# Performance work log

Hardware: AMD Instinct MI355X
Metric: run time of the kernel (lower is better)

## Reference

```python
import jax, jax.numpy as jnp
import numpy as np
import math

B, S, D = 8, 4096, 768
H = 12
DH = D // H  # attention_head_size = 64


def setup_inputs() -> dict:
    key = jax.random.key(0)
    ks = jax.random.split(key, 6)
    sc = 0.02
    return {
        "hidden_states": jax.random.normal(ks[0], (B, S, D), dtype=jnp.float32),
        "attention_mask": jnp.zeros((B, 1, S), dtype=jnp.float32),
        "Wq": jax.random.normal(ks[1], (D, D), dtype=jnp.float32) * sc,
        "bq": jnp.zeros((D,), dtype=jnp.float32),
        "Wqa": jax.random.normal(ks[2], (H, D), dtype=jnp.float32) * sc,
        "bqa": jnp.zeros((H,), dtype=jnp.float32),
        "Wk": jax.random.normal(ks[3], (D, D), dtype=jnp.float32) * sc,
        "bk": jnp.zeros((D,), dtype=jnp.float32),
        "Wt": jax.random.normal(ks[4], (D, D), dtype=jnp.float32) * sc,
        "bt": jnp.zeros((D,), dtype=jnp.float32),
    }


def reference(hidden_states, attention_mask, Wq, bq, Wqa, bqa, Wk, bk, Wt, bt):
    inv_sqrt_dh = 1.0 / math.sqrt(DH)
    # projections (torch nn.Linear: x @ W.T + b)
    q = hidden_states @ Wq.T + bq            # [B,S,D]
    k = hidden_states @ Wk.T + bk            # [B,S,D]
    # query attention logits -> [B,H,S]
    qfs = jnp.swapaxes(q @ Wqa.T + bqa, 1, 2) * inv_sqrt_dh + attention_mask
    qw = jax.nn.softmax(qfs, axis=-1)        # [B,H,S]
    ql = jnp.swapaxes(q.reshape(B, S, H, DH), 1, 2)  # [B,H,S,DH]
    kl = jnp.swapaxes(k.reshape(B, S, H, DH), 1, 2)  # [B,H,S,DH]
    # global pooled query per head
    pooled_q = jnp.einsum('bhs,bhsd->bhd', qw, ql)   # [B,H,DH]
    # key attention over pooled query
    qks = jnp.einsum('bhsd,bhd->bhs', kl, pooled_q) * inv_sqrt_dh + attention_mask
    qkw = jax.nn.softmax(qks, axis=-1)       # [B,H,S]
    pooled_k = jnp.einsum('bhs,bhsd->bhd', qkw, kl)  # [B,H,DH]
    # gate query with pooled key, merge heads
    wv = pooled_k[:, :, None, :] * ql        # [B,H,S,DH]
    wv = jnp.swapaxes(wv, 1, 2).reshape(B, S, D)
    return wv @ Wt.T + bt + q
```

## Files before the change

kernel.cpp:

```cpp
#include <hip/hip_runtime.h>
#include <cstdint>
#include <cstddef>

#define S_LEN 4096
#define NB 8
#define NH 12
#define DMODEL 768
#define DHEAD 64
#define M_TOT (NB * S_LEN)
#define INV_SQRT_DH 0.125f
#define WSZ (DMODEL * DMODEL)

typedef __attribute__((ext_vector_type(4))) float f32x4;
typedef __attribute__((ext_vector_type(8))) short bf16x8;

__device__ inline float bf2f(unsigned short h) {
    union { unsigned int u; float f; } v; v.u = ((unsigned int)h) << 16; return v.f;
}
__device__ inline unsigned short f2bf(float f) {
    union { float f; unsigned int u; } v; v.f = f;
    unsigned int r = v.u + 0x7FFFu + ((v.u >> 16) & 1u);
    return (unsigned short)(r >> 16);
}

__device__ inline void gload_lds16(const unsigned short* gp, void* lp) {
    __builtin_amdgcn_global_load_lds((const __attribute__((address_space(1))) void*)gp,
                                     (__attribute__((address_space(3))) void*)lp,
                                     16, 0, 0);
}

__global__ void prep_all(const float* __restrict__ hs,
                         const float* __restrict__ Wq, const float* __restrict__ Wk,
                         const float* __restrict__ Wt, const float* __restrict__ Wqa,
                         const float* __restrict__ bq, const float* __restrict__ bk,
                         unsigned short* __restrict__ hs_bf,
                         unsigned short* __restrict__ Wqk_bf, unsigned short* __restrict__ Wt_bf,
                         unsigned short* __restrict__ Wqa_bf, float* __restrict__ bqk) {
    int bid = blockIdx.x;
    int t = threadIdx.x;
    if (bid < 24576) {
        int off = bid * 1024 + t * 4;
        float4 v = *(const float4*)(hs + off);
        ushort4 o;
        o.x = f2bf(v.x); o.y = f2bf(v.y); o.z = f2bf(v.z); o.w = f2bf(v.w);
        *(ushort4*)(hs_bf + off) = o;
        return;
    }
    bid -= 24576;
    if (bid < 1728) {
        const float* src = (bid < 576) ? Wq : ((bid < 1152) ? Wk : Wt);
        unsigned short* dst = (bid < 576) ? Wqk_bf : ((bid < 1152) ? (Wqk_bf + WSZ) : Wt_bf);
        int off = (bid % 576) * 1024 + t * 4;
        float4 v = *(const float4*)(src + off);
        ushort4 o;
        o.x = f2bf(v.x); o.y = f2bf(v.y); o.z = f2bf(v.z); o.w = f2bf(v.w);
        *(ushort4*)(dst + off) = o;
    } else if (bid < 1740) {
        int off = (bid - 1728) * 1024 + t * 4;
        int h = off / DMODEL;
        ushort4 o = {0, 0, 0, 0};
        if (h < NH) {
            float4 v = *(const float4*)(Wqa + off);
            o.x = f2bf(v.x); o.y = f2bf(v.y); o.z = f2bf(v.z); o.w = f2bf(v.w);
        }
        *(ushort4*)(Wqa_bf + off) = o;
    } else {
        int off = (bid - 1740) * 1024 + t * 4;
        if (off < 2 * DMODEL) {
            const float* src = (off < DMODEL) ? (bq + off) : (bk + off - DMODEL);
            *(float4*)(bqk + off) = *(const float4*)src;
        }
    }
}

#define PH_MID() do { __builtin_amdgcn_s_barrier(); \
    asm volatile("s_waitcnt lgkmcnt(0)"); \
    __builtin_amdgcn_sched_barrier(0); \
    __builtin_amdgcn_s_setprio(1); } while (0)
#define PH_END() do { __builtin_amdgcn_s_setprio(0); \
    __builtin_amdgcn_s_barrier(); } while (0)

#define STG_A(q, kt, BO) gload_lds16(pA + (size_t)((q) * 64) * lda + (kt) * 64, \
                                     lds + (BO) + (q) * 8192 + wOff)
#define STG_B(q, kt, BO) gload_lds16(pB + (size_t)((q) * 64) * 768 + (kt) * 64, \
                                     lds + (BO) + 32768 + (q) * 8192 + wOff)

#define LD_A(mh, BO) do { _Pragma("unroll") for (int mm = 0; mm < 4; ++mm) { \
    a[mm][0] = *(const bf16x8*)(lds + (BO) + aRd0 + ((mh) * 4 + mm) * 2048); \
    a[mm][1] = *(const bf16x8*)(lds + (BO) + aRd1 + ((mh) * 4 + mm) * 2048); } } while (0)
#define LD_B(nh, BO) do { _Pragma("unroll") for (int nn = 0; nn < 2; ++nn) { \
    b[(nh) * 2 + nn][0] = *(const bf16x8*)(lds + (BO) + bRd0 + ((nh) * 2 + nn) * 2048); \
    b[(nh) * 2 + nn][1] = *(const bf16x8*)(lds + (BO) + bRd1 + ((nh) * 2 + nn) * 2048); } } while (0)
#define MFMAQ(mh, nh) do { _Pragma("unroll") for (int mm = 0; mm < 4; ++mm) \
    _Pragma("unroll") for (int nn = 0; nn < 2; ++nn) { \
        acc[(mh) * 4 + mm][(nh) * 2 + nn] = __builtin_amdgcn_mfma_f32_16x16x32_bf16( \
            a[mm][0], b[(nh) * 2 + nn][0], acc[(mh) * 4 + mm][(nh) * 2 + nn], 0, 0, 0); \
        acc[(mh) * 4 + mm][(nh) * 2 + nn] = __builtin_amdgcn_mfma_f32_16x16x32_bf16( \
            a[mm][1], b[(nh) * 2 + nn][1], acc[(mh) * 4 + mm][(nh) * 2 + nn], 0, 0, 0); } } while (0)

template<int MODE>
__global__ __launch_bounds__(512, 2) void gemm8(
    const unsigned short* __restrict__ A, int lda,
    const unsigned short* __restrict__ Bw,
    const float* __restrict__ bias,
    unsigned short* __restrict__ outBf, int ldoBf,
    float* __restrict__ outF,
    const unsigned short* __restrict__ resid, int ldr,
    int ntn)
{
    __shared__ __align__(16) char lds[131072];

    int nwg = gridDim.x;
    int bid = blockIdx.x;
    int cpx = nwg >> 3;
    int swz = (bid & 7) * cpx + (bid >> 3);
    int bidn = swz % ntn, bidm = swz / ntn;
    int m0 = bidm * 256, n0 = bidn * 256;

    if (MODE == 1) Bw += (size_t)(m0 >> 12) * WSZ;

    int t = threadIdx.x;
    int w = t >> 6, lane = t & 63;
    int lr = lane & 15, lk = lane >> 4;
    int wr = w >> 2, wc = w & 3;
    int wOff = w << 10;

    int srow = t >> 3;
    int sblk = (t & 7) ^ (srow & 7);
    const unsigned short* pA = A + (size_t)(m0 + srow) * lda + sblk * 8;
    const unsigned short* pB = Bw + (size_t)(n0 + srow) * 768 + sblk * 8;

    int sx = lr & 7;
    int aRd0 = (wr * 128 + lr) * 128 + ((0 + lk) ^ sx) * 16;
    int aRd1 = (wr * 128 + lr) * 128 + ((4 + lk) ^ sx) * 16;
    int bRd0 = 32768 + (wc * 64 + lr) * 128 + ((0 + lk) ^ sx) * 16;
    int bRd1 = 32768 + (wc * 64 + lr) * 128 + ((4 + lk) ^ sx) * 16;

    f32x4 acc[8][4];
#pragma unroll
    for (int m = 0; m < 8; ++m)
#pragma unroll
        for (int n = 0; n < 4; ++n)
            acc[m][n] = (f32x4){0.f, 0.f, 0.f, 0.f};
    bf16x8 a[4][2], b[4][2];

    STG_A(0, 0, 0); STG_A(1, 0, 0); STG_A(2, 0, 0); STG_A(3, 0, 0);
    STG_B(0, 0, 0); STG_B(1, 0, 0); STG_B(2, 0, 0); STG_B(3, 0, 0);
    STG_A(0, 1, 65536); STG_A(2, 1, 65536);
    STG_B(0, 1, 65536); STG_B(1, 1, 65536); STG_B(2, 1, 65536); STG_B(3, 1, 65536);
    asm volatile("s_waitcnt vmcnt(6)");
    __builtin_amdgcn_s_barrier();

    for (int i = 0; i < 6; ++i) {
        int ktE = 2 * i, ktO = 2 * i + 1;
        int s2 = (i < 5);
        LD_A(0, 0); LD_B(0, 0);
        STG_A(1, ktO, 65536); STG_A(3, ktO, 65536);
        PH_MID(); MFMAQ(0, 0); PH_END();
        LD_B(1, 0);
        if (s2) { STG_A(0, ktE + 2, 0); STG_A(2, ktE + 2, 0); }
        PH_MID(); MFMAQ(0, 1); PH_END();
        LD_A(1, 0);
        if (s2) { STG_B(0, ktE + 2, 0); STG_B(1, ktE + 2, 0); }
        PH_MID(); MFMAQ(1, 1); PH_END();
        if (s2) { STG_B(2, ktE + 2, 0); STG_B(3, ktE + 2, 0); }
        PH_MID(); MFMAQ(1, 0);
        __builtin_amdgcn_s_setprio(0);
        if (s2) { asm volatile("s_waitcnt vmcnt(6)"); }
        else    { asm volatile("s_waitcnt vmcnt(0)"); }
        __builtin_amdgcn_s_barrier();
        LD_A(0, 65536); LD_B(0, 65536);
        if (s2) { STG_A(1, ktE + 2, 0); STG_A(3, ktE + 2, 0); }
        PH_MID(); MFMAQ(0, 0); PH_END();
        LD_B(1, 65536);
        if (s2) { STG_A(0, ktO + 2, 65536); STG_A(2, ktO + 2, 65536); }
        PH_MID(); MFMAQ(0, 1); PH_END();
        LD_A(1, 65536);
        if (s2) { STG_B(0, ktO + 2, 65536); STG_B(1, ktO + 2, 65536); }
        PH_MID(); MFMAQ(1, 1); PH_END();
        if (s2) { STG_B(2, ktO + 2, 65536); STG_B(3, ktO + 2, 65536); }
        PH_MID(); MFMAQ(1, 0);
        __builtin_amdgcn_s_setprio(0);
        if (s2) { asm volatile("s_waitcnt vmcnt(6)"); }
        __builtin_amdgcn_s_barrier();
    }

#pragma unroll
    for (int m = 0; m < 8; ++m) {
        int gr0 = m0 + wr * 128 + m * 16 + lk * 4;
#pragma unroll
        for (int n = 0; n < 4; ++n) {
            int gc = n0 + wc * 64 + n * 16 + lr;
            float bv = bias[gc];
#pragma unroll
            for (int r = 0; r < 4; ++r) {
                int gr = gr0 + r;
                float v = acc[m][n][r] + bv;
                if (MODE == 0) {
                    outBf[(size_t)gr * ldoBf + gc] = f2bf(v);
                } else {
                    v += bf2f(resid[(size_t)gr * ldr + gc]);
                    outF[(size_t)gr * DMODEL + gc] = v;
                }
            }
        }
    }
}

__global__ __launch_bounds__(256) void qfs_kernel(
    const unsigned short* __restrict__ q, int ldq,
    const unsigned short* __restrict__ wqa,
    const float* __restrict__ bqa,
    const float* __restrict__ mask,
    float* __restrict__ qfs)
{
    int t = threadIdx.x;
    int w = t >> 6, lane = t & 63;
    int lr = lane & 15, lk = lane >> 4;
    int m0 = blockIdx.x * 64 + w * 16;

    f32x4 acc = (f32x4){0.f, 0.f, 0.f, 0.f};
    for (int k0 = 0; k0 < DMODEL; k0 += 32) {
        bf16x8 av = *(const bf16x8*)&q[(size_t)(m0 + lr) * ldq + k0 + lk * 8];
        bf16x8 bv = *(const bf16x8*)&wqa[lr * DMODEL + k0 + lk * 8];
        acc = __builtin_amdgcn_mfma_f32_16x16x32_bf16(av, bv, acc, 0, 0, 0);
    }
    if (lr < NH) {
        float bv = bqa[lr];
#pragma unroll
        for (int r = 0; r < 4; ++r) {
            int m = m0 + lk * 4 + r;
            int b_ = m >> 12;
            int s = m & (S_LEN - 1);
            qfs[((size_t)b_ * NH + lr) * S_LEN + s] = acc[r] * INV_SQRT_DH + bv + mask[b_ * S_LEN + s];
        }
    }
}

__global__ __launch_bounds__(256) void pool1_kernel(
    const float* __restrict__ logits,
    const unsigned short* __restrict__ qk,
    float* __restrict__ parts)
{
    int bid = blockIdx.x;
    int bh = bid >> 3, c = bid & 7;
    int b = bh / NH, h = bh % NH;
    int s0 = c * 512;
    int t = threadIdx.x;

    __shared__ float w[512];
    __shared__ float red[8];
    __shared__ float part[4][64];

    const float* lg = logits + (size_t)bh * S_LEN + s0;
    float l0 = lg[t], l1 = lg[t + 256];
    float m = fmaxf(l0, l1);
#pragma unroll
    for (int off = 32; off; off >>= 1) m = fmaxf(m, __shfl_xor(m, off));
    if ((t & 63) == 0) red[t >> 6] = m;
    __syncthreads();
    float M = fmaxf(fmaxf(red[0], red[1]), fmaxf(red[2], red[3]));
    float w0 = __expf(l0 - M), w1 = __expf(l1 - M);
    w[t] = w0; w[t + 256] = w1;
    float z = w0 + w1;
#pragma unroll
    for (int off = 32; off; off >>= 1) z += __shfl_xor(z, off);
    if ((t & 63) == 0) red[4 + (t >> 6)] = z;
    __syncthreads();
    float Z = red[4] + red[5] + red[6] + red[7];

    int dblk = t & 7, rgrp = t >> 3;
    const unsigned short* xp = qk + ((size_t)(b * S_LEN + s0)) * 1536 + h * DHEAD + dblk * 8;
    float acc[8];
#pragma unroll
    for (int e = 0; e < 8; ++e) acc[e] = 0.f;
    for (int j = 0; j < 16; ++j) {
        int r = j * 32 + rgrp;
        bf16x8 v = *(const bf16x8*)(xp + (size_t)r * 1536);
        float wr = w[r];
#pragma unroll
        for (int e = 0; e < 8; ++e) acc[e] += wr * bf2f((unsigned short)v[e]);
    }
#pragma unroll
    for (int off = 8; off <= 32; off <<= 1)
#pragma unroll
        for (int e = 0; e < 8; ++e) acc[e] += __shfl_xor(acc[e], off);
    if ((t & 63) < 8) {
#pragma unroll
        for (int e = 0; e < 8; ++e) part[t >> 6][(t & 7) * 8 + e] = acc[e];
    }
    __syncthreads();
    float* dst = parts + ((size_t)bh * 8 + c) * 72;
    if (t < 64) dst[t] = part[0][t] + part[1][t] + part[2][t] + part[3][t];
    else if (t == 64) dst[64] = M;
    else if (t == 65) dst[65] = Z;
}

__global__ __launch_bounds__(256) void pool2_kernel(
    const float* __restrict__ parts1,
    const unsigned short* __restrict__ qk,
    const float* __restrict__ mask,
    float* __restrict__ parts2)
{
    int bid = blockIdx.x;
    int bh = bid >> 3, c = bid & 7;
    int b = bh / NH, h = bh % NH;
    int s0 = c * 512;
    int t = threadIdx.x;

    __shared__ float pq[64];
    __shared__ float w[512];
    __shared__ float red[8];
    __shared__ float part[4][64];

    if (t < 64) {
        const float* p1 = parts1 + (size_t)bh * 8 * 72;
        float M1 = -1e30f;
#pragma unroll
        for (int cc = 0; cc < 8; ++cc) M1 = fmaxf(M1, p1[cc * 72 + 64]);
        float Z1 = 0.f, a1 = 0.f;
#pragma unroll
        for (int cc = 0; cc < 8; ++cc) {
            float f = __expf(p1[cc * 72 + 64] - M1);
            Z1 += f * p1[cc * 72 + 65];
            a1 += f * p1[cc * 72 + t];
        }
        pq[t] = a1 / Z1;
    }
    __syncthreads();

    int dblk = t & 7, rgrp = t >> 3;
    float pq8[8];
#pragma unroll
    for (int e = 0; e < 8; ++e) pq8[e] = pq[dblk * 8 + e];

    const unsigned short* kp = qk + ((size_t)(b * S_LEN + s0)) * 1536 + DMODEL + h * DHEAD + dblk * 8;

    for (int j = 0; j < 16; ++j) {
        int r = j * 32 + rgrp;
        bf16x8 v = *(const bf16x8*)(kp + (size_t)r * 1536);
        float d = 0.f;
#pragma unroll
        for (int e = 0; e < 8; ++e) d += bf2f((unsigned short)v[e]) * pq8[e];
        d += __shfl_xor(d, 1); d += __shfl_xor(d, 2); d += __shfl_xor(d, 4);
        if (dblk == 0) w[r] = d * INV_SQRT_DH + mask[b * S_LEN + s0 + r];
    }
    __syncthreads();

    float l0 = w[t], l1 = w[t + 256];
    float m = fmaxf(l0, l1);
#pragma unroll
    for (int off = 32; off; off >>= 1) m = fmaxf(m, __shfl_xor(m, off));
    if ((t & 63) == 0) red[t >> 6] = m;
    __syncthreads();
    float M = fmaxf(fmaxf(red[0], red[1]), fmaxf(red[2], red[3]));
    float w0 = __expf(l0 - M), w1 = __expf(l1 - M);
    float z = w0 + w1;
#pragma unroll
    for (int off = 32; off; off >>= 1) z += __shfl_xor(z, off);
    if ((t & 63) == 0) red[4 + (t >> 6)] = z;
    __syncthreads();
    w[t] = w0; w[t + 256] = w1;
    __syncthreads();
    float Z = red[4] + red[5] + red[6] + red[7];

    float acc[8];
#pragma unroll
    for (int e = 0; e < 8; ++e) acc[e] = 0.f;
    for (int j = 0; j < 16; ++j) {
        int r = j * 32 + rgrp;
        bf16x8 v = *(const bf16x8*)(kp + (size_t)r * 1536);
        float wr = w[r];
#pragma unroll
        for (int e = 0; e < 8; ++e) acc[e] += wr * bf2f((unsigned short)v[e]);
    }
#pragma unroll
    for (int off = 8; off <= 32; off <<= 1)
#pragma unroll
        for (int e = 0; e < 8; ++e) acc[e] += __shfl_xor(acc[e], off);
    if ((t & 63) < 8) {
#pragma unroll
        for (int e = 0; e < 8; ++e) part[t >> 6][(t & 7) * 8 + e] = acc[e];
    }
    __syncthreads();
    float* dst = parts2 + ((size_t)bh * 8 + c) * 72;
    if (t < 64) dst[t] = part[0][t] + part[1][t] + part[2][t] + part[3][t];
    else if (t == 64) dst[64] = M;
    else if (t == 65) dst[65] = Z;
}

__global__ __launch_bounds__(256) void gatedw_kernel(
    const float* __restrict__ parts2,
    const unsigned short* __restrict__ Wt_bf,
    unsigned short* __restrict__ W8)
{
    int bid = blockIdx.x;
    int b = bid / 96, rg = bid % 96;
    int t = threadIdx.x;

    __shared__ float mhc[96], Mh[12], fac[96], zh[12], pk[768];

    if (t < 96) mhc[t] = parts2[((size_t)(b * NH + t / 8) * 8 + (t & 7)) * 72 + 64];
    __syncthreads();
    if (t < 12) {
        float M = -1e30f;
#pragma unroll
        for (int cc = 0; cc < 8; ++cc) M = fmaxf(M, mhc[t * 8 + cc]);
        Mh[t] = M;
    }
    __syncthreads();
    if (t < 96) fac[t] = __expf(mhc[t] - Mh[t / 8]);
    __syncthreads();
    if (t < 12) {
        float Zm = 0.f;
#pragma unroll
        for (int cc = 0; cc < 8; ++cc)
            Zm += fac[t * 8 + cc] * parts2[((size_t)(b * NH + t) * 8 + cc) * 72 + 65];
        zh[t] = Zm;
    }
    __syncthreads();
#pragma unroll
    for (int j = 0; j < 3; ++j) {
        int col = t + 256 * j;
        int h = col >> 6, d = col & 63;
        const float* p2 = parts2 + (size_t)(b * NH + h) * 8 * 72;
        float v = 0.f;
#pragma unroll
        for (int cc = 0; cc < 8; ++cc) v += fac[h * 8 + cc] * p2[cc * 72 + d];
        pk[col] = v / zh[h];
    }
    __syncthreads();
#pragma unroll
    for (int j = 0; j < 3; ++j) {
        int idx = j * 2048 + t * 8;
        int r = rg * 8 + idx / DMODEL, k = idx % DMODEL;
        bf16x8 wv = *(const bf16x8*)(Wt_bf + (size_t)r * DMODEL + k);
        bf16x8 o;
#pragma unroll
        for (int e = 0; e < 8; ++e)
            o[e] = (short)f2bf(bf2f((unsigned short)wv[e]) * pk[k + e]);
        *(bf16x8*)(W8 + (size_t)b * WSZ + (size_t)r * DMODEL + k) = o;
    }
}

extern "C" void kernel_launch(void* const* d_in, const int* in_sizes, int n_in,
                              void* d_out, int out_size, void* d_ws, size_t ws_size,
                              hipStream_t stream) {
    const float* hs   = (const float*)d_in[0];
    const float* mask = (const float*)d_in[1];
    const float* Wq   = (const float*)d_in[2];
    const float* bq   = (const float*)d_in[3];
    const float* Wqa  = (const float*)d_in[4];
    const float* bqa  = (const float*)d_in[5];
    const float* Wk   = (const float*)d_in[6];
    const float* bk   = (const float*)d_in[7];
    const float* Wt   = (const float*)d_in[8];
    const float* bt   = (const float*)d_in[9];
    float* out = (float*)d_out;

    char* ws = (char*)d_ws;
    unsigned short* qk_bf  = (unsigned short*)(ws);
    unsigned short* hs_bf  = (unsigned short*)(ws + 100663296);
    unsigned short* W8     = hs_bf;
    unsigned short* Wqk_bf = (unsigned short*)(ws + 150994944);
    unsigned short* Wt_bf  = (unsigned short*)(ws + 153354240);
    unsigned short* Wqa_bf = (unsigned short*)(ws + 154533888);
    float* bqk    = (float*)(ws + 154558464);
    float* qfs    = (float*)(ws + 154564608);
    float* parts1 = (float*)(ws + 156137472);
    float* parts2 = (float*)(ws + 156358656);

    prep_all<<<26318, 256, 0, stream>>>(hs, Wq, Wk, Wt, Wqa, bq, bk,
                                        hs_bf, Wqk_bf, Wt_bf, Wqa_bf, bqk);

    gemm8<0><<<(M_TOT / 256) * 6, 512, 0, stream>>>(
        hs_bf, DMODEL, Wqk_bf, bqk, qk_bf, 2 * DMODEL, nullptr, nullptr, 0, 6);

    qfs_kernel<<<M_TOT / 64, 256, 0, stream>>>(qk_bf, 2 * DMODEL, Wqa_bf, bqa, mask, qfs);

    pool1_kernel<<<NB * NH * 8, 256, 0, stream>>>(qfs, qk_bf, parts1);
    pool2_kernel<<<NB * NH * 8, 256, 0, stream>>>(parts1, qk_bf, mask, parts2);
    gatedw_kernel<<<NB * 96, 256, 0, stream>>>(parts2, Wt_bf, W8);

    gemm8<1><<<(M_TOT / 256) * 3, 512, 0, stream>>>(
        qk_bf, 2 * DMODEL, W8, bt, nullptr, 0, out, qk_bf, 2 * DMODEL, 3);
}
```

Baseline: 222.5 us.

## Fuse query-logit computation with first pooling and retile output GEMM to 256x128

Merges the qfs logit kernel and pool1 into one kernel that computes the per-64-row logits, does a local softmax and a weighted partial pooled-query sum, and writes per-block partials. pool2 now merges 64 partials per batch-head instead of 8. The final GEMM gets its own kernel with 256x128 tiles and a smaller LDS footprint, which doubles the block count from 384 to 768 for better CU occupancy. The intent is to remove the qfs buffer round trip and one launch, at the cost of more serial partial-merging work in pool2.

```diff
diff --git a/kernel.cpp b/kernel.cpp
--- a/kernel.cpp
+++ b/kernel.cpp
@@ -80,7 +80,7 @@
 #define PH_END() do { __builtin_amdgcn_s_setprio(0); \
     __builtin_amdgcn_s_barrier(); } while (0)
 
-#define STG_A(q, kt, BO) gload_lds16(pA + (size_t)((q) * 64) * lda + (kt) * 64, \
+#define STG_A(q, kt, BO) gload_lds16(pA + (size_t)((q) * 64) * 768 + (kt) * 64, \
                                      lds + (BO) + (q) * 8192 + wOff)
 #define STG_B(q, kt, BO) gload_lds16(pB + (size_t)((q) * 64) * 768 + (kt) * 64, \
                                      lds + (BO) + 32768 + (q) * 8192 + wOff)
@@ -98,14 +98,11 @@
         acc[(mh) * 4 + mm][(nh) * 2 + nn] = __builtin_amdgcn_mfma_f32_16x16x32_bf16( \
             a[mm][1], b[(nh) * 2 + nn][1], acc[(mh) * 4 + mm][(nh) * 2 + nn], 0, 0, 0); } } while (0)
 
-template<int MODE>
 __global__ __launch_bounds__(512, 2) void gemm8(
-    const unsigned short* __restrict__ A, int lda,
+    const unsigned short* __restrict__ A,
     const unsigned short* __restrict__ Bw,
     const float* __restrict__ bias,
     unsigned short* __restrict__ outBf, int ldoBf,
-    float* __restrict__ outF,
-    const unsigned short* __restrict__ resid, int ldr,
     int ntn)
 {
     __shared__ __align__(16) char lds[131072];
@@ -117,8 +114,6 @@
     int bidn = swz % ntn, bidm = swz / ntn;
     int m0 = bidm * 256, n0 = bidn * 256;
 
-    if (MODE == 1) Bw += (size_t)(m0 >> 12) * WSZ;
-
     int t = threadIdx.x;
     int w = t >> 6, lane = t & 63;
     int lr = lane & 15, lk = lane >> 4;
@@ -127,7 +122,7 @@
 
     int srow = t >> 3;
     int sblk = (t & 7) ^ (srow & 7);
-    const unsigned short* pA = A + (size_t)(m0 + srow) * lda + sblk * 8;
+    const unsigned short* pA = A + (size_t)(m0 + srow) * 768 + sblk * 8;
     const unsigned short* pB = Bw + (size_t)(n0 + srow) * 768 + sblk * 8;
 
     int sx = lr & 7;
@@ -195,33 +190,152 @@
 #pragma unroll
             for (int r = 0; r < 4; ++r) {
                 int gr = gr0 + r;
-                float v = acc[m][n][r] + bv;
-                if (MODE == 0) {
-                    outBf[(size_t)gr * ldoBf + gc] = f2bf(v);
-                } else {
-                    v += bf2f(resid[(size_t)gr * ldr + gc]);
-                    outF[(size_t)gr * DMODEL + gc] = v;
-                }
+                outBf[(size_t)gr * ldoBf + gc] = f2bf(acc[m][n][r] + bv);
             }
         }
     }
 }
 
-__global__ __launch_bounds__(256) void qfs_kernel(
-    const unsigned short* __restrict__ q, int ldq,
+#define STG2_A(q, kt, BO) gload_lds16(pA + (size_t)((q) * 64) * 1536 + (kt) * 64, \
+                                      lds + (BO) + (q) * 8192 + wOff)
+#define STG2_B(q, kt, BO) gload_lds16(pB + (size_t)((q) * 64) * 768 + (kt) * 64, \
+                                      lds + (BO) + 32768 + (q) * 8192 + wOff)
+#define LD2_A(mp, BO) do { _Pragma("unroll") for (int mm = 0; mm < 2; ++mm) { \
+    a[mm][0] = *(const bf16x8*)(lds + (BO) + aRd0 + (2 * (mp) + mm) * 2048); \
+    a[mm][1] = *(const bf16x8*)(lds + (BO) + aRd1 + (2 * (mp) + mm) * 2048); } } while (0)
+#define LD2_B(BO) do { _Pragma("unroll") for (int nn = 0; nn < 2; ++nn) { \
+    b[nn][0] = *(const bf16x8*)(lds + (BO) + bRd0 + (nn) * 2048); \
+    b[nn][1] = *(const bf16x8*)(lds + (BO) + bRd1 + (nn) * 2048); } } while (0)
+#define MFMA2(mp) do { _Pragma("unroll") for (int mm = 0; mm < 2; ++mm) \
+    _Pragma("unroll") for (int nn = 0; nn < 2; ++nn) { \
+        acc[2 * (mp) + mm][nn] = __builtin_amdgcn_mfma_f32_16x16x32_bf16( \
+            a[mm][0], b[nn][0], acc[2 * (mp) + mm][nn], 0, 0, 0); \
+        acc[2 * (mp) + mm][nn] = __builtin_amdgcn_mfma_f32_16x16x32_bf16( \
+            a[mm][1], b[nn][1], acc[2 * (mp) + mm][nn], 0, 0, 0); } } while (0)
+
+__global__ __launch_bounds__(512, 2) void gemm8b(
+    const unsigned short* __restrict__ A,
+    const unsigned short* __restrict__ W8,
+    const float* __restrict__ bias,
+    float* __restrict__ outF,
+    const unsigned short* __restrict__ resid)
+{
+    __shared__ __align__(16) char lds[98304];
+
+    int nwg = gridDim.x;
+    int bid = blockIdx.x;
+    int cpx = nwg >> 3;
+    int swz = (bid & 7) * cpx + (bid >> 3);
+    int bidn = swz % 6, bidm = swz / 6;
+    int m0 = bidm * 256, n0 = bidn * 128;
+
+    const unsigned short* Bw = W8 + (size_t)(m0 >> 12) * WSZ;
+
+    int t = threadIdx.x;
+    int w = t >> 6, lane = t & 63;
+    int lr = lane & 15, lk = lane >> 4;
+    int wr = w >> 2, wc = w & 3;
+    int wOff = w << 10;
+
+    int srow = t >> 3;
+    int sblk = (t & 7) ^ (srow & 7);
+    const unsigned short* pA = A + (size_t)(m0 + srow) * 1536 + sblk * 8;
+    const unsigned short* pB = Bw + (size_t)(n0 + srow) * 768 + sblk * 8;
+
+    int sx = lr & 7;
+    int aRd0 = (wr * 128 + lr) * 128 + ((0 + lk) ^ sx) * 16;
+    int aRd1 = (wr * 128 + lr) * 128 + ((4 + lk) ^ sx) * 16;
+    int bRd0 = 32768 + (wc * 32 + lr) * 128 + ((0 + lk) ^ sx) * 16;
+    int bRd1 = 32768 + (wc * 32 + lr) * 128 + ((4 + lk) ^ sx) * 16;
+
+    f32x4 acc[8][2];
+#pragma unroll
+    for (int m = 0; m < 8; ++m)
+#pragma unroll
+        for (int n = 0; n < 2; ++n)
+            acc[m][n] = (f32x4){0.f, 0.f, 0.f, 0.f};
+    bf16x8 a[2][2], b[2][2];
+
+    STG2_A(0, 0, 0); STG2_A(1, 0, 0); STG2_A(2, 0, 0); STG2_A(3, 0, 0);
+    STG2_B(0, 0, 0); STG2_B(1, 0, 0);
+    STG2_A(0, 1, 49152); STG2_A(2, 1, 49152);
+    STG2_B(0, 1, 49152); STG2_B(1, 1, 49152);
+    asm volatile("s_waitcnt vmcnt(4)");
+    __builtin_amdgcn_s_barrier();
+
+    for (int i = 0; i < 6; ++i) {
+        int ktE = 2 * i, ktO = 2 * i + 1;
+        int s2 = (i < 5);
+        LD2_A(0, 0); LD2_B(0);
+        STG2_A(1, ktO, 49152); STG2_A(3, ktO, 49152);
+        PH_MID(); MFMA2(0); PH_END();
+        LD2_A(1, 0);
+        PH_MID(); MFMA2(1); PH_END();
+        LD2_A(2, 0);
+        if (s2) { STG2_A(0, ktE + 2, 0); STG2_A(2, ktE + 2, 0); }
+        PH_MID(); MFMA2(2); PH_END();
+        LD2_A(3, 0);
+        if (s2) { STG2_B(0, ktE + 2, 0); STG2_B(1, ktE + 2, 0); }
+        PH_MID(); MFMA2(3);
+        __builtin_amdgcn_s_setprio(0);
+        if (s2) { asm volatile("s_waitcnt vmcnt(4)"); }
+        else    { asm volatile("s_waitcnt vmcnt(0)"); }
+        __builtin_amdgcn_s_barrier();
+        LD2_A(0, 49152); LD2_B(49152);
+        if (s2) { STG2_A(1, ktE + 2, 0); STG2_A(3, ktE + 2, 0); }
+        PH_MID(); MFMA2(0); PH_END();
+        LD2_A(1, 49152);
+        PH_MID(); MFMA2(1); PH_END();
+        LD2_A(2, 49152);
+        if (s2) { STG2_A(0, ktO + 2, 49152); STG2_A(2, ktO + 2, 49152); }
+        PH_MID(); MFMA2(2); PH_END();
+        LD2_A(3, 49152);
+        if (s2) { STG2_B(0, ktO + 2, 49152); STG2_B(1, ktO + 2, 49152); }
+        PH_MID(); MFMA2(3);
+        __builtin_amdgcn_s_setprio(0);
+        if (s2) { asm volatile("s_waitcnt vmcnt(4)"); }
+        __builtin_amdgcn_s_barrier();
+    }
+
+#pragma unroll
+    for (int m = 0; m < 8; ++m) {
+        int gr0 = m0 + wr * 128 + m * 16 + lk * 4;
+#pragma unroll
+        for (int n = 0; n < 2; ++n) {
+            int gc = n0 + wc * 32 + n * 16 + lr;
+            float bv = bias[gc];
+#pragma unroll
+            for (int r = 0; r < 4; ++r) {
+                int gr = gr0 + r;
+                float v = acc[m][n][r] + bv + bf2f(resid[(size_t)gr * 1536 + gc]);
+                outF[(size_t)gr * DMODEL + gc] = v;
+            }
+        }
+    }
+}
+
+__global__ __launch_bounds__(256) void qfspool_kernel(
+    const unsigned short* __restrict__ q,
     const unsigned short* __restrict__ wqa,
     const float* __restrict__ bqa,
     const float* __restrict__ mask,
-    float* __restrict__ qfs)
+    float* __restrict__ parts1)
 {
+    int bid = blockIdx.x;
+    int m0 = bid * 64;
+    int b = m0 >> 12;
     int t = threadIdx.x;
     int w = t >> 6, lane = t & 63;
     int lr = lane & 15, lk = lane >> 4;
-    int m0 = blockIdx.x * 64 + w * 16;
+    int m0w = m0 + w * 16;
+
+    __shared__ float lgt[16][68];
+    __shared__ float mz[12], zz[12];
+    __shared__ float pl[12][2][64];
 
     f32x4 acc = (f32x4){0.f, 0.f, 0.f, 0.f};
     for (int k0 = 0; k0 < DMODEL; k0 += 32) {
-        bf16x8 av = *(const bf16x8*)&q[(size_t)(m0 + lr) * ldq + k0 + lk * 8];
+        bf16x8 av = *(const bf16x8*)&q[(size_t)(m0w + lr) * 1536 + k0 + lk * 8];
         bf16x8 bv = *(const bf16x8*)&wqa[lr * DMODEL + k0 + lk * 8];
         acc = __builtin_amdgcn_mfma_f32_16x16x32_bf16(av, bv, acc, 0, 0, 0);
     }
@@ -229,71 +343,56 @@
         float bv = bqa[lr];
 #pragma unroll
         for (int r = 0; r < 4; ++r) {
-            int m = m0 + lk * 4 + r;
-            int b_ = m >> 12;
-            int s = m & (S_LEN - 1);
-            qfs[((size_t)b_ * NH + lr) * S_LEN + s] = acc[r] * INV_SQRT_DH + bv + mask[b_ * S_LEN + s];
-        }
-    }
-}
-
-__global__ __launch_bounds__(256) void pool1_kernel(
-    const float* __restrict__ logits,
-    const unsigned short* __restrict__ qk,
-    float* __restrict__ parts)
-{
-    int bid = blockIdx.x;
-    int bh = bid >> 3, c = bid & 7;
-    int b = bh / NH, h = bh % NH;
-    int s0 = c * 512;
-    int t = threadIdx.x;
-
-    __shared__ float w[512];
-    __shared__ float red[8];
-    __shared__ float part[4][64];
-
-    const float* lg = logits + (size_t)bh * S_LEN + s0;
-    float l0 = lg[t], l1 = lg[t + 256];
-    float m = fmaxf(l0, l1);
-#pragma unroll
-    for (int off = 32; off; off >>= 1) m = fmaxf(m, __shfl_xor(m, off));
-    if ((t & 63) == 0) red[t >> 6] = m;
-    __syncthreads();
-    float M = fmaxf(fmaxf(red[0], red[1]), fmaxf(red[2], red[3]));
-    float w0 = __expf(l0 - M), w1 = __expf(l1 - M);
-    w[t] = w0; w[t + 256] = w1;
-    float z = w0 + w1;
-#pragma unroll
-    for (int off = 32; off; off >>= 1) z += __shfl_xor(z, off);
-    if ((t & 63) == 0) red[4 + (t >> 6)] = z;
-    __syncthreads();
-    float Z = red[4] + red[5] + red[6] + red[7];
-
-    int dblk = t & 7, rgrp = t >> 3;
-    const unsigned short* xp = qk + ((size_t)(b * S_LEN + s0)) * 1536 + h * DHEAD + dblk * 8;
-    float acc[8];
-#pragma unroll
-    for (int e = 0; e < 8; ++e) acc[e] = 0.f;
-    for (int j = 0; j < 16; ++j) {
-        int r = j * 32 + rgrp;
-        bf16x8 v = *(const bf16x8*)(xp + (size_t)r * 1536);
-        float wr = w[r];
-#pragma unroll
-        for (int e = 0; e < 8; ++e) acc[e] += wr * bf2f((unsigned short)v[e]);
-    }
-#pragma unroll
-    for (int off = 8; off <= 32; off <<= 1)
-#pragma unroll
-        for (int e = 0; e < 8; ++e) acc[e] += __shfl_xor(acc[e], off);
-    if ((t & 63) < 8) {
-#pragma unroll
-        for (int e = 0; e < 8; ++e) part[t >> 6][(t & 7) * 8 + e] = acc[e];
-    }
-    __syncthreads();
-    float* dst = parts + ((size_t)bh * 8 + c) * 72;
-    if (t < 64) dst[t] = part[0][t] + part[1][t] + part[2][t] + part[3][t];
-    else if (t == 64) dst[64] = M;
-    else if (t == 65) dst[65] = Z;
+            int row = w * 16 + lk * 4 + r;
+            lgt[lr][row] = acc[r] * INV_SQRT_DH + bv + mask[b * S_LEN + ((m0 + row) & (S_LEN - 1))];
+        }
+    }
+    __syncthreads();
+
+    if (t < 192) {
+        int h = t >> 4, idx = t & 15;
+        float v0 = lgt[h][idx * 4 + 0], v1 = lgt[h][idx * 4 + 1];
+        float v2 = lgt[h][idx * 4 + 2], v3 = lgt[h][idx * 4 + 3];
+        float m = fmaxf(fmaxf(v0, v1), fmaxf(v2, v3));
+        m = fmaxf(m, __shfl_xor(m, 1)); m = fmaxf(m, __shfl_xor(m, 2));
+        m = fmaxf(m, __shfl_xor(m, 4)); m = fmaxf(m, __shfl_xor(m, 8));
+        float e0 = __expf(v0 - m), e1 = __expf(v1 - m), e2 = __expf(v2 - m), e3 = __expf(v3 - m);
+        lgt[h][idx * 4 + 0] = e0; lgt[h][idx * 4 + 1] = e1;
+        lgt[h][idx * 4 + 2] = e2; lgt[h][idx * 4 + 3] = e3;
+        float z = e0 + e1 + e2 + e3;
+        z += __shfl_xor(z, 1); z += __shfl_xor(z, 2);
+        z += __shfl_xor(z, 4); z += __shfl_xor(z, 8);
+        if (idx == 0) { mz[h] = m; zz[h] = z; }
+    }
+    __syncthreads();
+
+    if (t < 192) {
+        int h = t >> 4, sub = t & 15, oct = sub >> 1, rg = sub & 1;
+        const unsigned short* xp = q + (size_t)(m0 + rg * 32) * 1536 + h * DHEAD + oct * 8;
+        float a8[8];
+#pragma unroll
+        for (int e = 0; e < 8; ++e) a8[e] = 0.f;
+        for (int r = 0; r < 32; ++r) {
+            float wg = lgt[h][rg * 32 + r];
+            bf16x8 v = *(const bf16x8*)(xp + (size_t)r * 1536);
+#pragma unroll
+            for (int e = 0; e < 8; ++e) a8[e] += wg * bf2f((unsigned short)v[e]);
+        }
+#pragma unroll
+        for (int e = 0; e < 8; ++e) pl[h][rg][oct * 8 + e] = a8[e];
+    }
+    __syncthreads();
+
+    float* dst = parts1 + (size_t)bid * 12 * 66;
+    if (t < 192) {
+        int h = t >> 4, idx = t & 15;
+#pragma unroll
+        for (int j = 0; j < 4; ++j) {
+            int d = idx * 4 + j;
+            dst[h * 66 + d] = pl[h][0][d] + pl[h][1][d];
+        }
+        if (idx == 0) { dst[h * 66 + 64] = mz[h]; dst[h * 66 + 65] = zz[h]; }
+    }
 }
 
 __global__ __launch_bounds__(256) void pool2_kernel(
@@ -314,16 +413,15 @@
     __shared__ float part[4][64];
 
     if (t < 64) {
-        const float* p1 = parts1 + (size_t)bh * 8 * 72;
         float M1 = -1e30f;
-#pragma unroll
-        for (int cc = 0; cc < 8; ++cc) M1 = fmaxf(M1, p1[cc * 72 + 64]);
+        for (int cc = 0; cc < 64; ++cc)
+            M1 = fmaxf(M1, parts1[((size_t)(b * 64 + cc) * 12 + h) * 66 + 64]);
         float Z1 = 0.f, a1 = 0.f;
-#pragma unroll
-        for (int cc = 0; cc < 8; ++cc) {
-            float f = __expf(p1[cc * 72 + 64] - M1);
-            Z1 += f * p1[cc * 72 + 65];
-            a1 += f * p1[cc * 72 + t];
+        for (int cc = 0; cc < 64; ++cc) {
+            const float* p1 = parts1 + ((size_t)(b * 64 + cc) * 12 + h) * 66;
+            float f = __expf(p1[64] - M1);
+            Z1 += f * p1[65];
+            a1 += f * p1[t];
         }
         pq[t] = a1 / Z1;
     }
@@ -466,22 +564,19 @@
     unsigned short* Wt_bf  = (unsigned short*)(ws + 153354240);
     unsigned short* Wqa_bf = (unsigned short*)(ws + 154533888);
     float* bqk    = (float*)(ws + 154558464);
-    float* qfs    = (float*)(ws + 154564608);
-    float* parts1 = (float*)(ws + 156137472);
-    float* parts2 = (float*)(ws + 156358656);
+    float* parts1 = (float*)(ws + 154564608);
+    float* parts2 = (float*)(ws + 156186624);
 
     prep_all<<<26318, 256, 0, stream>>>(hs, Wq, Wk, Wt, Wqa, bq, bk,
                                         hs_bf, Wqk_bf, Wt_bf, Wqa_bf, bqk);
 
-    gemm8<0><<<(M_TOT / 256) * 6, 512, 0, stream>>>(
-        hs_bf, DMODEL, Wqk_bf, bqk, qk_bf, 2 * DMODEL, nullptr, nullptr, 0, 6);
-
-    qfs_kernel<<<M_TOT / 64, 256, 0, stream>>>(qk_bf, 2 * DMODEL, Wqa_bf, bqa, mask, qfs);
-
-    pool1_kernel<<<NB * NH * 8, 256, 0, stream>>>(qfs, qk_bf, parts1);
+    gemm8<<<(M_TOT / 256) * 6, 512, 0, stream>>>(
+        hs_bf, Wqk_bf, bqk, qk_bf, 2 * DMODEL, 6);
+
+    qfspool_kernel<<<M_TOT / 64, 256, 0, stream>>>(qk_bf, Wqa_bf, bqa, mask, parts1);
     pool2_kernel<<<NB * NH * 8, 256, 0, stream>>>(parts1, qk_bf, mask, parts2);
     gatedw_kernel<<<NB * 96, 256, 0, stream>>>(parts2, Wt_bf, W8);
 
-    gemm8<1><<<(M_TOT / 256) * 3, 512, 0, stream>>>(
-        qk_bf, 2 * DMODEL, W8, bt, nullptr, 0, out, qk_bf, 2 * DMODEL, 3);
-}
+    gemm8b<<<(M_TOT / 256) * 6, 512, 0, stream>>>(
+        qk_bf, W8, bt, out, qk_bf);
+}
```

Result: slower. 228.5 us (+2.7%).

## Specialize output GEMM with 256x128 tiles and triple-buffered LDS pipeline

Applied to the files above, without the earlier changes.

The templated GEMM is split into two kernels: the Q/K projection keeps the 256x256 tile with the row stride hardcoded, and the final output GEMM gets a dedicated kernel with 256x128 tiles and triple-buffered LDS staging. The output grid doubles to 768 blocks so the 256 CUs are better filled, and the extra buffer lets loads run two k-tiles ahead. The cost is more A-tile reloads per output column and larger LDS use (144KB), which may limit occupancy.

```diff
diff --git a/kernel.cpp b/kernel.cpp
--- a/kernel.cpp
+++ b/kernel.cpp
@@ -80,7 +80,7 @@
 #define PH_END() do { __builtin_amdgcn_s_setprio(0); \
     __builtin_amdgcn_s_barrier(); } while (0)
 
-#define STG_A(q, kt, BO) gload_lds16(pA + (size_t)((q) * 64) * lda + (kt) * 64, \
+#define STG_A(q, kt, BO) gload_lds16(pA + (size_t)((q) * 64) * 768 + (kt) * 64, \
                                      lds + (BO) + (q) * 8192 + wOff)
 #define STG_B(q, kt, BO) gload_lds16(pB + (size_t)((q) * 64) * 768 + (kt) * 64, \
                                      lds + (BO) + 32768 + (q) * 8192 + wOff)
@@ -98,14 +98,11 @@
         acc[(mh) * 4 + mm][(nh) * 2 + nn] = __builtin_amdgcn_mfma_f32_16x16x32_bf16( \
             a[mm][1], b[(nh) * 2 + nn][1], acc[(mh) * 4 + mm][(nh) * 2 + nn], 0, 0, 0); } } while (0)
 
-template<int MODE>
 __global__ __launch_bounds__(512, 2) void gemm8(
-    const unsigned short* __restrict__ A, int lda,
+    const unsigned short* __restrict__ A,
     const unsigned short* __restrict__ Bw,
     const float* __restrict__ bias,
     unsigned short* __restrict__ outBf, int ldoBf,
-    float* __restrict__ outF,
-    const unsigned short* __restrict__ resid, int ldr,
     int ntn)
 {
     __shared__ __align__(16) char lds[131072];
@@ -117,8 +114,6 @@
     int bidn = swz % ntn, bidm = swz / ntn;
     int m0 = bidm * 256, n0 = bidn * 256;
 
-    if (MODE == 1) Bw += (size_t)(m0 >> 12) * WSZ;
-
     int t = threadIdx.x;
     int w = t >> 6, lane = t & 63;
     int lr = lane & 15, lk = lane >> 4;
@@ -127,7 +122,7 @@
 
     int srow = t >> 3;
     int sblk = (t & 7) ^ (srow & 7);
-    const unsigned short* pA = A + (size_t)(m0 + srow) * lda + sblk * 8;
+    const unsigned short* pA = A + (size_t)(m0 + srow) * 768 + sblk * 8;
     const unsigned short* pB = Bw + (size_t)(n0 + srow) * 768 + sblk * 8;
 
     int sx = lr & 7;
@@ -195,13 +190,112 @@
 #pragma unroll
             for (int r = 0; r < 4; ++r) {
                 int gr = gr0 + r;
-                float v = acc[m][n][r] + bv;
-                if (MODE == 0) {
-                    outBf[(size_t)gr * ldoBf + gc] = f2bf(v);
-                } else {
-                    v += bf2f(resid[(size_t)gr * ldr + gc]);
-                    outF[(size_t)gr * DMODEL + gc] = v;
-                }
+                outBf[(size_t)gr * ldoBf + gc] = f2bf(acc[m][n][r] + bv);
+            }
+        }
+    }
+}
+
+#define STG3_A(q, kt, BO) gload_lds16(pA + (size_t)((q) * 64) * 1536 + (kt) * 64, \
+                                      lds + (BO) + (q) * 8192 + wOff)
+#define STG3_B(q, kt, BO) gload_lds16(pB + (size_t)((q) * 64) * 768 + (kt) * 64, \
+                                      lds + (BO) + 32768 + (q) * 8192 + wOff)
+#define LD3_A(mlo, BO) do { _Pragma("unroll") for (int mm = 0; mm < 4; ++mm) { \
+    a[mm][0] = *(const bf16x8*)(lds + (BO) + aRd0 + ((mlo) + mm) * 2048); \
+    a[mm][1] = *(const bf16x8*)(lds + (BO) + aRd1 + ((mlo) + mm) * 2048); } } while (0)
+#define LD3_B(BO) do { _Pragma("unroll") for (int nn = 0; nn < 2; ++nn) { \
+    b[nn][0] = *(const bf16x8*)(lds + (BO) + bRd0 + (nn) * 2048); \
+    b[nn][1] = *(const bf16x8*)(lds + (BO) + bRd1 + (nn) * 2048); } } while (0)
+#define MFMA3(mlo) do { _Pragma("unroll") for (int mm = 0; mm < 4; ++mm) \
+    _Pragma("unroll") for (int nn = 0; nn < 2; ++nn) { \
+        acc[(mlo) + mm][nn] = __builtin_amdgcn_mfma_f32_16x16x32_bf16( \
+            a[mm][0], b[nn][0], acc[(mlo) + mm][nn], 0, 0, 0); \
+        acc[(mlo) + mm][nn] = __builtin_amdgcn_mfma_f32_16x16x32_bf16( \
+            a[mm][1], b[nn][1], acc[(mlo) + mm][nn], 0, 0, 0); } } while (0)
+
+#define TILE3(t, BO, SO) do { \
+    int t2 = (t) + 2; int s2 = (t2 < 12); \
+    LD3_A(0, BO); LD3_B(BO); \
+    if (s2) { STG3_A(0, t2, SO); STG3_A(1, t2, SO); STG3_A(2, t2, SO); } \
+    PH_MID(); MFMA3(0); PH_END(); \
+    LD3_A(4, BO); \
+    if (s2) { STG3_A(3, t2, SO); STG3_B(0, t2, SO); STG3_B(1, t2, SO); } \
+    PH_MID(); MFMA3(4); \
+    __builtin_amdgcn_s_setprio(0); \
+    if ((t) <= 9) { asm volatile("s_waitcnt vmcnt(6)"); } \
+    else if ((t) == 10) { asm volatile("s_waitcnt vmcnt(0)"); } \
+    __builtin_amdgcn_s_barrier(); \
+} while (0)
+
+__global__ __launch_bounds__(512, 2) void gemm8b(
+    const unsigned short* __restrict__ A,
+    const unsigned short* __restrict__ W8,
+    const float* __restrict__ bias,
+    float* __restrict__ outF,
+    const unsigned short* __restrict__ resid)
+{
+    __shared__ __align__(16) char lds[147456];
+
+    int nwg = gridDim.x;
+    int bid = blockIdx.x;
+    int cpx = nwg >> 3;
+    int swz = (bid & 7) * cpx + (bid >> 3);
+    int bidn = swz % 6, bidm = swz / 6;
+    int m0 = bidm * 256, n0 = bidn * 128;
+
+    const unsigned short* Bw = W8 + (size_t)(m0 >> 12) * WSZ;
+
+    int t = threadIdx.x;
+    int w = t >> 6, lane = t & 63;
+    int lr = lane & 15, lk = lane >> 4;
+    int wr = w >> 2, wc = w & 3;
+    int wOff = w << 10;
+
+    int srow = t >> 3;
+    int sblk = (t & 7) ^ (srow & 7);
+    const unsigned short* pA = A + (size_t)(m0 + srow) * 1536 + sblk * 8;
+    const unsigned short* pB = Bw + (size_t)(n0 + srow) * 768 + sblk * 8;
+
+    int sx = lr & 7;
+    int aRd0 = (wr * 128 + lr) * 128 + ((0 + lk) ^ sx) * 16;
+    int aRd1 = (wr * 128 + lr) * 128 + ((4 + lk) ^ sx) * 16;
+    int bRd0 = 32768 + (wc * 32 + lr) * 128 + ((0 + lk) ^ sx) * 16;
+    int bRd1 = 32768 + (wc * 32 + lr) * 128 + ((4 + lk) ^ sx) * 16;
+
+    f32x4 acc[8][2];
+#pragma unroll
+    for (int m = 0; m < 8; ++m)
+#pragma unroll
+        for (int n = 0; n < 2; ++n)
+            acc[m][n] = (f32x4){0.f, 0.f, 0.f, 0.f};
+    bf16x8 a[4][2], b[2][2];
+
+    STG3_A(0, 0, 0); STG3_A(1, 0, 0); STG3_A(2, 0, 0); STG3_A(3, 0, 0);
+    STG3_B(0, 0, 0); STG3_B(1, 0, 0);
+    STG3_A(0, 1, 49152); STG3_A(1, 1, 49152); STG3_A(2, 1, 49152); STG3_A(3, 1, 49152);
+    STG3_B(0, 1, 49152); STG3_B(1, 1, 49152);
+    asm volatile("s_waitcnt vmcnt(6)");
+    __builtin_amdgcn_s_barrier();
+
+    for (int ii = 0; ii < 4; ++ii) {
+        int tb = ii * 3;
+        TILE3(tb + 0, 0,     98304);
+        TILE3(tb + 1, 49152, 0);
+        TILE3(tb + 2, 98304, 49152);
+    }
+
+#pragma unroll
+    for (int m = 0; m < 8; ++m) {
+        int gr0 = m0 + wr * 128 + m * 16 + lk * 4;
+#pragma unroll
+        for (int n = 0; n < 2; ++n) {
+            int gc = n0 + wc * 32 + n * 16 + lr;
+            float bv = bias[gc];
+#pragma unroll
+            for (int r = 0; r < 4; ++r) {
+                int gr = gr0 + r;
+                float v = acc[m][n][r] + bv + bf2f(resid[(size_t)gr * 1536 + gc]);
+                outF[(size_t)gr * DMODEL + gc] = v;
             }
         }
     }
@@ -473,15 +567,14 @@
     prep_all<<<26318, 256, 0, stream>>>(hs, Wq, Wk, Wt, Wqa, bq, bk,
                                         hs_bf, Wqk_bf, Wt_bf, Wqa_bf, bqk);
 
-    gemm8<0><<<(M_TOT / 256) * 6, 512, 0, stream>>>(
-        hs_bf, DMODEL, Wqk_bf, bqk, qk_bf, 2 * DMODEL, nullptr, nullptr, 0, 6);
+    gemm8<<<(M_TOT / 256) * 6, 512, 0, stream>>>(
+        hs_bf, Wqk_bf, bqk, qk_bf, 2 * DMODEL, 6);
 
     qfs_kernel<<<M_TOT / 64, 256, 0, stream>>>(qk_bf, 2 * DMODEL, Wqa_bf, bqa, mask, qfs);
-
     pool1_kernel<<<NB * NH * 8, 256, 0, stream>>>(qfs, qk_bf, parts1);
     pool2_kernel<<<NB * NH * 8, 256, 0, stream>>>(parts1, qk_bf, mask, parts2);
     gatedw_kernel<<<NB * 96, 256, 0, stream>>>(parts2, Wt_bf, W8);
 
-    gemm8<1><<<(M_TOT / 256) * 3, 512, 0, stream>>>(
-        qk_bf, 2 * DMODEL, W8, bt, nullptr, 0, out, qk_bf, 2 * DMODEL, 3);
-}
+    gemm8b<<<(M_TOT / 256) * 6, 512, 0, stream>>>(
+        qk_bf, W8, bt, out, qk_bf);
+}
```

New measurement: 215.6 us. -3.1%, faster.
